# Optimization experiments

Measured on AMD Instinct MI355X. Metric: run time of the kernel, lower is better.

## Reference

```python
import jax, jax.numpy as jnp
import numpy as np

DIM = 64        # output embedding dim
N_CHUNKS = 3
D = 4           # per-core dim = ceil(DIM ** (1/N_CHUNKS))
RANK = 16
HRANGE = 131072
BATCH = 131072


def setup_inputs() -> dict:
    key = jax.random.key(0)
    k_hs, k_s, k_e, k_c = jax.random.split(key, 4)
    hs = jax.random.randint(k_hs, (BATCH, N_CHUNKS), 0, HRANGE, dtype=jnp.int64)
    # init per reset_parameters (split_dim=True): scale = (d*rank)**-0.5 for cores/end,
    # start_core uniform in +-d**-0.5
    scale = (D * RANK) ** -0.5
    s0 = D ** -0.5
    start_core = jax.random.uniform(k_s, (HRANGE, D, RANK), jnp.float32, -s0, s0)
    end_core = jax.random.uniform(k_e, (HRANGE, D, RANK), jnp.float32, -scale, scale)
    cores = jax.random.uniform(k_c, (N_CHUNKS - 2, HRANGE, D, RANK, RANK), jnp.float32, -scale, scale)
    return {"hs": hs, "start_core": start_core, "end_core": end_core, "cores": cores}


def reference(hs, start_core, end_core, cores):
    B = hs.shape[0]
    # split_dim=True branch of TensorTrainEmbedding.forward
    v = end_core[hs[:, -1]]                      # [B, d, r]
    for i in range(hs.shape[1] - 2):             # fixed small loop over TT cores
        core = cores[i][hs[:, i + 1]]            # [B, d, r, r] irregular gather
        v = jnp.einsum('bdsr,ber->bdes', core, v)  # [B, d, e, r]
        v = v.reshape(B, -1, v.shape[-1])        # flatten(1,2) -> [B, d*e, r]
    v = jnp.einsum('bdr,ber->bde', start_core[hs[:, 0]], v)  # [B, d, e]
    v = v.reshape(B, -1)[:, :DIM]                # [B, dim]
    return v
```

## Files before the change

### kernel.cpp

```cpp
#include <hip/hip_runtime.h>


#define WPB 4
#define T_STRIDE 20

__global__ __launch_bounds__(256) void tt_embed_kernel(
    const int* __restrict__ hs,
    const float* __restrict__ start_core,
    const float* __restrict__ end_core,
    const float* __restrict__ cores,
    float* __restrict__ out,
    int B)
{
    __shared__ __align__(16) float lds_t[WPB][16 * T_STRIDE];

    const int tid  = threadIdx.x;
    const int wave = tid >> 6;
    const int lane = tid & 63;

    int b = blockIdx.x * WPB + wave;
    b = __builtin_amdgcn_readfirstlane(b);
    const bool active = (b < B);

    float st[16];
    float t[4];

    if (active) {
        const int h0 = __builtin_amdgcn_readfirstlane(hs[3 * b + 0]);
        const int h1 = __builtin_amdgcn_readfirstlane(hs[3 * b + 1]);
        const int h2 = __builtin_amdgcn_readfirstlane(hs[3 * b + 2]);

        const float* crp = cores + ((size_t)h1 << 10) + lane * 16;
        float c[16];
        *(float4*)(c + 0)  = *(const float4*)(crp + 0);
        *(float4*)(c + 4)  = *(const float4*)(crp + 4);
        *(float4*)(c + 8)  = *(const float4*)(crp + 8);
        *(float4*)(c + 12) = *(const float4*)(crp + 12);

        const float* stp = start_core + ((size_t)h0 << 6) + ((lane >> 4) << 4);
        *(float4*)(st + 0)  = *(const float4*)(stp + 0);
        *(float4*)(st + 4)  = *(const float4*)(stp + 4);
        *(float4*)(st + 8)  = *(const float4*)(stp + 8);
        *(float4*)(st + 12) = *(const float4*)(stp + 12);

        const float* v0p = end_core + ((size_t)h2 << 6);
        #pragma unroll
        for (int e = 0; e < 4; ++e) {
            const float* ve = v0p + e * 16;
            float a = c[0] * ve[0];
            #pragma unroll
            for (int r = 1; r < 16; ++r)
                a = fmaf(c[r], ve[r], a);
            t[e] = a;
        }

        const int d = lane >> 4;
        const int s = lane & 15;
        #pragma unroll
        for (int e = 0; e < 4; ++e)
            lds_t[wave][(d * 4 + e) * T_STRIDE + s] = t[e];
    }

    __syncthreads();

    if (active) {
        const float* tp = &lds_t[wave][(lane & 15) * T_STRIDE];
        float tt[16];
        *(float4*)(tt + 0)  = *(const float4*)(tp + 0);
        *(float4*)(tt + 4)  = *(const float4*)(tp + 4);
        *(float4*)(tt + 8)  = *(const float4*)(tp + 8);
        *(float4*)(tt + 12) = *(const float4*)(tp + 12);

        float a = st[0] * tt[0];
        #pragma unroll
        for (int k = 1; k < 16; ++k)
            a = fmaf(st[k], tt[k], a);

        out[((size_t)b << 6) + lane] = a;
    }
}

extern "C" void kernel_launch(void* const* d_in, const int* in_sizes, int n_in,
                              void* d_out, int out_size, void* d_ws, size_t ws_size,
                              hipStream_t stream) {
    const int*   hs         = (const int*)d_in[0];
    const float* start_core = (const float*)d_in[1];
    const float* end_core   = (const float*)d_in[2];
    const float* cores      = (const float*)d_in[3];
    float* out = (float*)d_out;

    const int B = in_sizes[0] / 3;
    const int grid = (B + WPB - 1) / WPB;

    hipLaunchKernelGGL(tt_embed_kernel, dim3(grid), dim3(256), 0, stream,
                       hs, start_core, end_core, cores, out, B);
}
```

Before: 95.64 us.

## Bucket-sort batch rows by middle-core index before the TT embedding kernel

Adds a histogram, scan and atomic scatter pass that builds a permutation of batch rows grouped by coarse bins of the h1 index. The main kernel then processes rows in that order, so gathers of the 4 KB middle cores hit nearby addresses and could get better cache and DRAM locality. In exchange it adds a memset, three extra launches, atomics and a single-block scan. Output writes become scattered, and the sorted path only runs when B equals the test batch size and the workspace is large enough.

```diff
diff --git a/kernel.cpp b/kernel.cpp
--- a/kernel.cpp
+++ b/kernel.cpp
@@ -3,12 +3,65 @@
 
 #define WPB 4
 #define T_STRIDE 20
+#define NBINS 4096
+#define BIN_SHIFT 5
+
+#define WS_HIST_OFF 0
+#define WS_OFFS_OFF (NBINS * 4)
+#define WS_PERM_OFF (2 * NBINS * 4)
+#define WS_NEEDED   (2 * NBINS * 4 + 131072 * 4)
+
+__global__ __launch_bounds__(256) void hist_kernel(
+    const int* __restrict__ hs, unsigned* __restrict__ hist, int B)
+{
+    int b = blockIdx.x * 256 + threadIdx.x;
+    if (b < B) {
+        unsigned h1 = (unsigned)hs[3 * b + 1];
+        atomicAdd(&hist[h1 >> BIN_SHIFT], 1u);
+    }
+}
+
+__global__ __launch_bounds__(256) void scan_kernel(
+    const unsigned* __restrict__ hist, unsigned* __restrict__ offs)
+{
+    __shared__ unsigned sums[256];
+    const int t = threadIdx.x;
+    unsigned local[16];
+    unsigned s = 0;
+    #pragma unroll
+    for (int i = 0; i < 16; ++i) { local[i] = hist[t * 16 + i]; s += local[i]; }
+    sums[t] = s;
+    __syncthreads();
+    #pragma unroll
+    for (int st = 1; st < 256; st <<= 1) {
+        unsigned v = (t >= st) ? sums[t - st] : 0u;
+        __syncthreads();
+        sums[t] += v;
+        __syncthreads();
+    }
+    unsigned run = sums[t] - s;
+    #pragma unroll
+    for (int i = 0; i < 16; ++i) { offs[t * 16 + i] = run; run += local[i]; }
+}
+
+__global__ __launch_bounds__(256) void scatter_kernel(
+    const int* __restrict__ hs, unsigned* __restrict__ offs,
+    unsigned* __restrict__ perm, int B)
+{
+    int b = blockIdx.x * 256 + threadIdx.x;
+    if (b < B) {
+        unsigned h1 = (unsigned)hs[3 * b + 1];
+        unsigned pos = atomicAdd(&offs[h1 >> BIN_SHIFT], 1u);
+        perm[pos] = (unsigned)b;
+    }
+}
 
 __global__ __launch_bounds__(256) void tt_embed_kernel(
     const int* __restrict__ hs,
     const float* __restrict__ start_core,
     const float* __restrict__ end_core,
     const float* __restrict__ cores,
+    const unsigned* __restrict__ perm,
     float* __restrict__ out,
     int B)
 {
@@ -18,9 +71,11 @@
     const int wave = tid >> 6;
     const int lane = tid & 63;
 
-    int b = blockIdx.x * WPB + wave;
+    int i = blockIdx.x * WPB + wave;
+    const bool active = (i < B);
+    int b = i;
+    if (active && perm) b = (int)perm[i];
     b = __builtin_amdgcn_readfirstlane(b);
-    const bool active = (b < B);
 
     float st[16];
     float t[4];
@@ -90,8 +145,28 @@
     float* out = (float*)d_out;
 
     const int B = in_sizes[0] / 3;
-    const int grid = (B + WPB - 1) / WPB;
+    const int grid_main = (B + WPB - 1) / WPB;
+    const int grid_b    = (B + 255) / 256;
 
-    hipLaunchKernelGGL(tt_embed_kernel, dim3(grid), dim3(256), 0, stream,
-                       hs, start_core, end_core, cores, out, B);
+    const bool use_sort = (ws_size >= (size_t)WS_NEEDED) && (B == 131072);
+
+    if (use_sort) {
+        unsigned* hist = (unsigned*)((char*)d_ws + WS_HIST_OFF);
+        unsigned* offs = (unsigned*)((char*)d_ws + WS_OFFS_OFF);
+        unsigned* perm = (unsigned*)((char*)d_ws + WS_PERM_OFF);
+
+        hipMemsetAsync(hist, 0, NBINS * 4, stream);
+        hipLaunchKernelGGL(hist_kernel, dim3(grid_b), dim3(256), 0, stream,
+                           hs, hist, B);
+        hipLaunchKernelGGL(scan_kernel, dim3(1), dim3(256), 0, stream,
+                           hist, offs);
+        hipLaunchKernelGGL(scatter_kernel, dim3(grid_b), dim3(256), 0, stream,
+                           hs, offs, perm, B);
+        hipLaunchKernelGGL(tt_embed_kernel, dim3(grid_main), dim3(256), 0, stream,
+                           hs, start_core, end_core, cores, perm, out, B);
+    } else {
+        hipLaunchKernelGGL(tt_embed_kernel, dim3(grid_main), dim3(256), 0, stream,
+                           hs, start_core, end_core, cores, (const unsigned*)nullptr,
+                           out, B);
+    }
 }
```

Result: slower. 121.8 us (+27.3%).
